# Kernel tuning notes

Measured on AMD Instinct MI355X. Metric: run time of the kernel, lower is better.

Reference implementation:

```python
import jax, jax.numpy as jnp
import numpy as np

N, K, IN, FEAT, H, OUT, E = 30000, 25, 64, 32, 128, 64, 480000


def setup_inputs() -> dict:
    key = jax.random.key(0)
    ks = jax.random.split(key, 24)
    w = lambda k, shp: (jax.random.normal(k, shp, dtype=jnp.float32) * 0.05)
    z = lambda n: jnp.zeros((n,), jnp.float32)
    return {
        "x": jax.random.normal(ks[0], (N, IN), jnp.float32),
        "dists_max": jax.random.uniform(ks[1], (N, K), jnp.float32),
        "dists_argmax": jax.random.randint(ks[2], (N, K), 0, N, jnp.int32),
        "edge_index": jax.random.randint(ks[3], (2, E), 0, N, jnp.int32),
        "train_mask": jnp.ones((E,), jnp.int32),
        # PGNN.linear_pre: in -> 32
        "w_pre": w(ks[4], (IN, FEAT)), "b_pre": z(FEAT),
        # conv_first (PGNN_layer(32, 128))
        "l1_dc_w1": w(ks[5], (1, H)), "l1_dc_b1": z(H),
        "l1_dc_w2": w(ks[6], (H, 1)), "l1_dc_b2": z(1),
        "l1_wh": w(ks[7], (2 * FEAT, H)), "l1_bh": z(H),
        "l1_wp": w(ks[8], (H, 1)), "l1_bp": z(1),
        # conv_out (PGNN_layer(128, 128))
        "l2_dc_w1": w(ks[9], (1, H)), "l2_dc_b1": z(H),
        "l2_dc_w2": w(ks[10], (H, 1)), "l2_dc_b2": z(1),
        "l2_wh": w(ks[11], (2 * H, H)), "l2_bh": z(H),
        "l2_wp": w(ks[12], (H, 1)), "l2_bp": z(1),
        # GNNModel.layers[1]: Linear(len_distmax=25 -> hidden=128)
        "w_lin": w(ks[13], (K, H)), "b_lin": z(H),
        # FeedForwardNetwork(2H -> 2H -> OUT)
        "ff_w1": w(ks[14], (2 * H, 2 * H)), "ff_b1": z(2 * H),
        "ff_w2": w(ks[15], (2 * H, OUT)), "ff_b2": z(OUT),
    }


def _nonlinear(d, w1, b1, w2, b2):
    # Nonlinear(1, H, 1) applied to dists: [N, K] -> [N, K]
    h = jax.nn.relu(d[..., None] @ w1 + b1)  # [N, K, H]
    return (h @ w2 + b2)[..., 0]


def _pgnn_layer(feat, dmax, argmax, dc_w1, dc_b1, dc_w2, dc_b2, wh, bh, wp, bp):
    d = _nonlinear(dmax, dc_w1, dc_b1, dc_w2, dc_b2)          # [N, K]
    sub = feat[argmax]                                         # gather: [N, K, F]
    self_feat = jnp.broadcast_to(feat[:, None, :], sub.shape)  # [N, K, F]
    msgs = jnp.concatenate([sub * d[..., None], self_feat], axis=-1)  # [N, K, 2F]
    msgs = jax.nn.relu(msgs @ wh + bh)                         # [N, K, H]
    out_position = (msgs @ wp + bp)[..., 0]                    # [N, K]
    out_structure = msgs.mean(axis=1)                          # [N, H]
    return out_position, out_structure


def reference(x, dists_max, dists_argmax, edge_index, train_mask,
              w_pre, b_pre,
              l1_dc_w1, l1_dc_b1, l1_dc_w2, l1_dc_b2, l1_wh, l1_bh, l1_wp, l1_bp,
              l2_dc_w1, l2_dc_b1, l2_dc_w2, l2_dc_b2, l2_wh, l2_bh, l2_wp, l2_bp,
              w_lin, b_lin, ff_w1, ff_b1, ff_w2, ff_b2):
    # PGNN (layer_num=2, feature_pre=True)
    h = x @ w_pre + b_pre                                      # [N, 32]
    _, h = _pgnn_layer(h, dists_max, dists_argmax,
                       l1_dc_w1, l1_dc_b1, l1_dc_w2, l1_dc_b2,
                       l1_wh, l1_bh, l1_wp, l1_bp)             # [N, H]
    x_pos, _ = _pgnn_layer(h, dists_max, dists_argmax,
                           l2_dc_w1, l2_dc_b1, l2_dc_w2, l2_dc_b2,
                           l2_wh, l2_bh, l2_wp, l2_bp)         # [N, K]
    # F.normalize(p=2, dim=-1) with eps=1e-12
    norm = jnp.maximum(jnp.linalg.norm(x_pos, axis=-1, keepdims=True), 1e-12)
    h = jax.nn.relu(x_pos / norm)                              # act after layer 0
    h = jax.nn.relu(h @ w_lin + b_lin)                         # layers[1] + act, [N, H]
    # get_minibatch_embeddings: select train edges, gather endpoint embeddings
    idx = np.where(np.asarray(train_mask) == 1)[0]
    ei = edge_index[:, idx]
    e = jnp.concatenate([h[ei[0]], h[ei[1]]], axis=1)          # [E_train, 2H]
    # FeedForwardNetwork
    e = jax.nn.relu(e @ ff_w1 + ff_b1)
    return e @ ff_w2 + ff_b2                                   # [E_train, OUT]
```

## Files before the change

### kernel.cpp

```cpp
#include <hip/hip_runtime.h>
#include <hip/hip_bf16.h>
#include <cmath>

#define NN 30000
#define KK 25
#define IN_F 64
#define FEAT 32
#define HH 128
#define OUTF 64
#define EE 480000
#define NPAGE 469
#define NB (8 * NPAGE)
#define LUTN 4096

typedef __attribute__((ext_vector_type(8))) _Float16 fp16x8;
typedef __attribute__((ext_vector_type(2))) _Float16 h2v;
typedef __attribute__((ext_vector_type(16))) float f32x16;

__device__ inline float u2f(unsigned u) { return __builtin_bit_cast(float, u); }
__device__ inline unsigned short f2b(float f) {
    __bf16 h = (__bf16)f;
    return __builtin_bit_cast(unsigned short, h);
}
__device__ inline unsigned short f2h(float f) {
    _Float16 h = (_Float16)f;
    return __builtin_bit_cast(unsigned short, h);
}
__device__ inline float blo(unsigned u) { return u2f(u << 16); }
__device__ inline float bhi(unsigned u) { return u2f(u & 0xffff0000u); }

__device__ inline unsigned hrelu2(unsigned a, unsigned b) {
    h2v x = __builtin_bit_cast(h2v, a);
    h2v y = __builtin_bit_cast(h2v, b);
    h2v s = x + y;
    h2v z = {(_Float16)0.f, (_Float16)0.f};
    h2v r = __builtin_elementwise_max(s, z);
    return __builtin_bit_cast(unsigned, r);
}

__device__ inline float lut_eval(const float* __restrict__ lut, float dm) {
    float tt = dm * (float)LUTN;
    int i0 = (int)tt;
    i0 = i0 < 0 ? 0 : (i0 > LUTN - 1 ? LUTN - 1 : i0);
    float f = tt - (float)i0;
    float l0 = lut[i0];
    return fmaf(lut[i0 + 1] - l0, f, l0);
}

__global__ void k_prep(const float* __restrict__ x,
                       const float* __restrict__ w_pre, const float* __restrict__ b_pre,
                       const float* __restrict__ l1wh, const float* __restrict__ l1bh,
                       const float* __restrict__ ffw2, const float* __restrict__ ffw1,
                       const float* __restrict__ l2wh,
                       const float* __restrict__ l1w1, const float* __restrict__ l1b1,
                       const float* __restrict__ l1w2, const float* __restrict__ l1b2,
                       const float* __restrict__ l2w1, const float* __restrict__ l2b1,
                       const float* __restrict__ l2w2, const float* __restrict__ l2b2,
                       unsigned* __restrict__ hist,
                       float* __restrict__ lut1, float* __restrict__ lut2,
                       unsigned short* __restrict__ xh, unsigned short* __restrict__ xl,
                       float* __restrict__ bfuse, unsigned short* __restrict__ wt,
                       unsigned short* __restrict__ wt1,
                       unsigned short* __restrict__ wt2h, unsigned short* __restrict__ wt2l,
                       unsigned short* __restrict__ wfh, unsigned short* __restrict__ wfl) {
    int gid = blockIdx.x * 256 + threadIdx.x;
    if (gid < NB) { hist[gid] = 0u; return; }
    gid -= NB;
    if (gid < 2 * (LUTN + 1)) {
        int which = gid / (LUTN + 1);
        int i = gid % (LUTN + 1);
        float dm = (float)i * (1.0f / (float)LUTN);
        const float* w1 = which ? l2w1 : l1w1;
        const float* b1 = which ? l2b1 : l1b1;
        const float* w2 = which ? l2w2 : l1w2;
        const float* b2 = which ? l2b2 : l1b2;
        float a = 0.f;
        for (int h = 0; h < HH; ++h)
            a = fmaf(fmaxf(fmaf(dm, w1[h], b1[h]), 0.f), w2[h], a);
        (which ? lut2 : lut1)[i] = a + b2[0];
        return;
    }
    gid -= 2 * (LUTN + 1);
    if (gid < NN * IN_F / 8) {
        int i = gid * 8;
        unsigned short vh[8], vl[8];
#pragma unroll
        for (int j = 0; j < 8; ++j) {
            float v = x[i + j];
            _Float16 hi = (_Float16)v;
            vh[j] = __builtin_bit_cast(unsigned short, hi);
            vl[j] = f2h((v - (float)hi) * 1024.f);
        }
        *(uint4*)(xh + i) = *(uint4*)vh;
        *(uint4*)(xl + i) = *(uint4*)vl;
        return;
    }
    gid -= NN * IN_F / 8;
    if (gid < 256) {
        int half = gid >> 7, h = gid & 127;
        const float* wh = l1wh + half * FEAT * HH + h;
        float acc = (half == 1) ? l1bh[h] : 0.f;
#pragma unroll
        for (int c = 0; c < FEAT; ++c) acc = fmaf(b_pre[c], wh[c * HH], acc);
        bfuse[gid] = acc;
    } else if (gid < 16640) {
        int i = gid - 256;
        int k = i >> 6, c = i & 63;
        wt[c * 256 + k] = f2h(ffw2[i]);
    } else if (gid < 82176) {
        int i = gid - 16640;
        int c = i >> 7, j = i & 127;
        float v = (c < 256) ? ffw1[j * 256 + c] : ffw1[(128 + j) * 256 + (c - 256)];
        wt1[c * 128 + j] = f2h(v);
    } else if (gid < 114944) {
        int i = gid - 82176;
        int c = i >> 7, j = i & 127;
        float v = (c < 128) ? l2wh[j * 128 + c] : l2wh[(128 + j) * 128 + (c - 128)];
        _Float16 hi = (_Float16)v;
        wt2h[c * 128 + j] = __builtin_bit_cast(unsigned short, hi);
        wt2l[c * 128 + j] = f2h((v - (float)hi) * 1024.f);
    } else if (gid < 131328) {
        int i = gid - 114944;
        int cc = i >> 6, j = i & 63;
        const float* wrow = w_pre + j * FEAT;
        float acc = 0.f;
#pragma unroll
        for (int c = 0; c < FEAT; ++c) {
            float wh = (cc < 128) ? l1wh[c * HH + cc] : l1wh[(FEAT + c) * HH + (cc - 128)];
            acc = fmaf(wrow[c], wh, acc);
        }
        _Float16 hi = (_Float16)acc;
        wfh[cc * 64 + j] = __builtin_bit_cast(unsigned short, hi);
        wfl[cc * 64 + j] = f2h((acc - (float)hi) * 1024.f);
    }
}

__global__ void k_dlut(const float* __restrict__ dmax, const float* __restrict__ lut1,
                       const float* __restrict__ lut2,
                       float* __restrict__ d1, float* __restrict__ d2) {
    int i = (blockIdx.x * 256 + threadIdx.x) * 4;
    if (i >= NN * KK) return;
    float4 dm = *(const float4*)(dmax + i);
    float4 o1, o2;
    o1.x = lut_eval(lut1, dm.x); o1.y = lut_eval(lut1, dm.y);
    o1.z = lut_eval(lut1, dm.z); o1.w = lut_eval(lut1, dm.w);
    o2.x = lut_eval(lut2, dm.x); o2.y = lut_eval(lut2, dm.y);
    o2.z = lut_eval(lut2, dm.z); o2.w = lut_eval(lut2, dm.w);
    *(float4*)(d1 + i) = o1;
    *(float4*)(d2 + i) = o2;
}

__global__ void k_hist(const int* __restrict__ ei, unsigned* __restrict__ hist) {
    int base = (blockIdx.x * 256 + threadIdx.x) * 8;
    if (base >= EE) return;
    int4 s0 = *(const int4*)(ei + base);
    int4 s1 = *(const int4*)(ei + base + 4);
    int4 d0 = *(const int4*)(ei + EE + base);
    int4 d1 = *(const int4*)(ei + EE + base + 4);
    int ss[8] = {s0.x, s0.y, s0.z, s0.w, s1.x, s1.y, s1.z, s1.w};
    int dd[8] = {d0.x, d0.y, d0.z, d0.w, d1.x, d1.y, d1.z, d1.w};
#pragma unroll
    for (int j = 0; j < 8; ++j) {
        int key = (ss[j] * 8 / NN) * NPAGE + (dd[j] >> 6);
        atomicAdd(&hist[key], 1u);
    }
}

__global__ __launch_bounds__(64) void k_scan(const unsigned* __restrict__ hist,
                                             unsigned* __restrict__ cursor) {
    int l = threadIdx.x;
    const int PER = 59;
    unsigned tot = 0;
    for (int j = 0; j < PER; ++j) {
        int i = l * PER + j;
        if (i < NB) tot += hist[i];
    }
    unsigned run = tot;
#pragma unroll
    for (int off = 1; off < 64; off <<= 1) {
        unsigned u = __shfl_up(run, off, 64);
        if (l >= off) run += u;
    }
    unsigned base = run - tot;
    for (int j = 0; j < PER; ++j) {
        int i = l * PER + j;
        if (i < NB) {
            cursor[i] = base;
            base += hist[i];
        }
    }
}

__global__ void k_scatter(const int* __restrict__ ei, unsigned* __restrict__ cursor,
                          uint4* __restrict__ sedge) {
    int base = (blockIdx.x * 256 + threadIdx.x) * 8;
    if (base >= EE) return;
    int4 s0 = *(const int4*)(ei + base);
    int4 s1 = *(const int4*)(ei + base + 4);
    int4 d0 = *(const int4*)(ei + EE + base);
    int4 d1 = *(const int4*)(ei + EE + base + 4);
    int ss[8] = {s0.x, s0.y, s0.z, s0.w, s1.x, s1.y, s1.z, s1.w};
    int dd[8] = {d0.x, d0.y, d0.z, d0.w, d1.x, d1.y, d1.z, d1.w};
    unsigned pp[8];
#pragma unroll
    for (int j = 0; j < 8; ++j) {
        int key = (ss[j] * 8 / NN) * NPAGE + (dd[j] >> 6);
        pp[j] = atomicAdd(&cursor[key], 1u);
    }
#pragma unroll
    for (int j = 0; j < 8; ++j)
        sedge[pp[j]] = make_uint4((unsigned)ss[j], (unsigned)dd[j], (unsigned)(base + j), 0u);
}

template <int KD>
__global__ __launch_bounds__(256) void k_nodegemm(
    const unsigned short* __restrict__ Ah, const unsigned short* __restrict__ Al,
    const unsigned short* __restrict__ Wh, const unsigned short* __restrict__ Wl,
    const float* __restrict__ gbias, const float* __restrict__ sbias,
    unsigned short* __restrict__ Gb, float* __restrict__ S) {
    int t = threadIdx.x;
    int l = t & 63, w = t >> 6;
    int c = l & 31, kh = l >> 5;
    int nb = blockIdx.x * 32;
    int na = nb + c;
    if (na >= NN) na = NN - 1;
    fp16x8 afh[KD / 16], afl[KD / 16];
#pragma unroll
    for (int kt = 0; kt < KD / 16; ++kt) {
        afh[kt] = *(const fp16x8*)(Ah + na * KD + kt * 16 + kh * 8);
        afl[kt] = *(const fp16x8*)(Al + na * KD + kt * 16 + kh * 8);
    }
    f32x16 acch0, acch1, accl0, accl1;
#pragma unroll
    for (int i = 0; i < 16; ++i) { acch0[i] = 0.f; acch1[i] = 0.f; accl0[i] = 0.f; accl1[i] = 0.f; }
    int cb0 = w * 64, cb1 = w * 64 + 32;
#pragma unroll
    for (int kt = 0; kt < KD / 16; ++kt) {
        fp16x8 b0h = *(const fp16x8*)(Wh + (cb0 + c) * KD + kt * 16 + kh * 8);
        fp16x8 b0l = *(const fp16x8*)(Wl + (cb0 + c) * KD + kt * 16 + kh * 8);
        fp16x8 b1h = *(const fp16x8*)(Wh + (cb1 + c) * KD + kt * 16 + kh * 8);
        fp16x8 b1l = *(const fp16x8*)(Wl + (cb1 + c) * KD + kt * 16 + kh * 8);
        acch0 = __builtin_amdgcn_mfma_f32_32x32x16_f16(afh[kt], b0h, acch0, 0, 0, 0);
        accl0 = __builtin_amdgcn_mfma_f32_32x32x16_f16(afh[kt], b0l, accl0, 0, 0, 0);
        accl0 = __builtin_amdgcn_mfma_f32_32x32x16_f16(afl[kt], b0h, accl0, 0, 0, 0);
        acch1 = __builtin_amdgcn_mfma_f32_32x32x16_f16(afh[kt], b1h, acch1, 0, 0, 0);
        accl1 = __builtin_amdgcn_mfma_f32_32x32x16_f16(afh[kt], b1l, accl1, 0, 0, 0);
        accl1 = __builtin_amdgcn_mfma_f32_32x32x16_f16(afl[kt], b1h, accl1, 0, 0, 0);
    }
    const float inv1024 = 1.0f / 1024.0f;
#pragma unroll
    for (int half = 0; half < 2; ++half) {
        int col = (half ? cb1 : cb0) + c;
        bool isG = col < HH;
        float gb_ = (isG && gbias) ? gbias[col] : 0.f;
        float sb_ = (!isG) ? sbias[col - HH] : 0.f;
#pragma unroll
        for (int r = 0; r < 16; ++r) {
            int row = (r & 3) + 8 * (r >> 2) + 4 * kh;
            int n = nb + row;
            float v = half ? (acch1[r] + accl1[r] * inv1024)
                           : (acch0[r] + accl0[r] * inv1024);
            if (n < NN) {
                if (isG) Gb[n * HH + col] = f2b(v + gb_);
                else S[n * HH + (col - HH)] = v + sb_;
            }
        }
    }
}

__global__ void k_layer1(const unsigned* __restrict__ G1u, const float* __restrict__ S1,
                         const float* __restrict__ d1, const int* __restrict__ amax,
                         unsigned* __restrict__ hh, unsigned* __restrict__ hl) {
    int t = threadIdx.x;
    int n = blockIdx.x * 4 + (t >> 6);
    int l = t & 63;
    float2 sv = *(const float2*)(S1 + n * HH + 2 * l);
    const int* arow = amax + n * KK;
    const float* drow = d1 + n * KK;
    unsigned gvv[KK];
#pragma unroll
    for (int k = 0; k < KK; ++k) gvv[k] = G1u[arow[k] * 64 + l];
    float dk_[KK];
#pragma unroll
    for (int k = 0; k < KK; ++k) dk_[k] = drow[k];
    float acc0 = 0.f, acc1 = 0.f;
#pragma unroll
    for (int k = 0; k < KK; ++k) {
        acc0 += fmaxf(fmaf(dk_[k], blo(gvv[k]), sv.x), 0.f);
        acc1 += fmaxf(fmaf(dk_[k], bhi(gvv[k]), sv.y), 0.f);
    }
    float a0 = acc0 * 0.04f, a1 = acc1 * 0.04f;
    _Float16 h0 = (_Float16)a0, h1v = (_Float16)a1;
    float r0 = (a0 - (float)h0) * 1024.f, r1 = (a1 - (float)h1v) * 1024.f;
    hh[n * 64 + l] = (unsigned)__builtin_bit_cast(unsigned short, h0) |
                     ((unsigned)__builtin_bit_cast(unsigned short, h1v) << 16);
    hl[n * 64 + l] = (unsigned)f2h(r0) | ((unsigned)f2h(r1) << 16);
}

__global__ __launch_bounds__(256) void k_xpos2(
    const uint2* __restrict__ G2u2, const float* __restrict__ S2,
    const float* __restrict__ d2, const int* __restrict__ amax,
    const float* __restrict__ wp, const float* __restrict__ bp,
    const float* __restrict__ wlin, const float* __restrict__ blin,
    uint2* __restrict__ hlu2) {
    int t = threadIdx.x;
    int s = t & 31;
    int n = blockIdx.x * 8 + (t >> 5);
    float4 sv = *(const float4*)(S2 + n * HH + 4 * s);
    float4 wpv = *(const float4*)(wp + 4 * s);
    const int* arow = amax + n * KK;
    const float* drow = d2 + n * KK;
    uint2 gvv[KK];
#pragma unroll
    for (int k = 0; k < KK; ++k) gvv[k] = G2u2[(size_t)arow[k] * 32 + s];
    float dk_[KK];
#pragma unroll
    for (int k = 0; k < KK; ++k) dk_[k] = drow[k];
    float v[KK];
#pragma unroll
    for (int k = 0; k < KK; ++k) {
        float d = dk_[k];
        float t0 = fmaxf(fmaf(d, blo(gvv[k].x), sv.x), 0.f);
        float t1 = fmaxf(fmaf(d, bhi(gvv[k].x), sv.y), 0.f);
        float t2 = fmaxf(fmaf(d, blo(gvv[k].y), sv.z), 0.f);
        float t3 = fmaxf(fmaf(d, bhi(gvv[k].y), sv.w), 0.f);
        v[k] = t0 * wpv.x + t1 * wpv.y + t2 * wpv.z + t3 * wpv.w;
    }
#pragma unroll
    for (int sh = 1; sh < 32; sh <<= 1) {
#pragma unroll
        for (int k = 0; k < KK; ++k) v[k] += __shfl_xor(v[k], sh, 64);
    }
    float bpv = bp[0];
    float ss = 0.f;
#pragma unroll
    for (int k = 0; k < KK; ++k) { v[k] += bpv; ss = fmaf(v[k], v[k], ss); }
    float inv = 1.0f / fmaxf(sqrtf(ss), 1e-12f);
    float4 bl = *(const float4*)(blin + 4 * s);
    float a0 = bl.x, a1 = bl.y, a2 = bl.z, a3 = bl.w;
#pragma unroll
    for (int k = 0; k < KK; ++k) {
        float xv = fmaxf(v[k], 0.f) * inv;
        float4 wl = *(const float4*)(wlin + k * HH + 4 * s);
        a0 = fmaf(xv, wl.x, a0);
        a1 = fmaf(xv, wl.y, a1);
        a2 = fmaf(xv, wl.z, a2);
        a3 = fmaf(xv, wl.w, a3);
    }
    uint2 o;
    o.x = (unsigned)f2h(fmaxf(a0, 0.f)) | ((unsigned)f2h(fmaxf(a1, 0.f)) << 16);
    o.y = (unsigned)f2h(fmaxf(a2, 0.f)) | ((unsigned)f2h(fmaxf(a3, 0.f)) << 16);
    hlu2[(size_t)n * 32 + s] = o;
}

__global__ __launch_bounds__(256) void k_ab_mfma(
    const unsigned short* __restrict__ hl16, const unsigned short* __restrict__ wt1,
    const float* __restrict__ ffb1, unsigned short* __restrict__ ab) {
    int t = threadIdx.x;
    int l = t & 63, w = t >> 6;
    int c = l & 31, kh = l >> 5;
    int nb = blockIdx.x * 32;
    int na = nb + c;
    if (na >= NN) na = NN - 1;
    fp16x8 af[8];
#pragma unroll
    for (int kt = 0; kt < 8; ++kt)
        af[kt] = *(const fp16x8*)(hl16 + na * 128 + kt * 16 + kh * 8);
    f32x16 acc[4];
#pragma unroll
    for (int g = 0; g < 4; ++g)
#pragma unroll
        for (int i = 0; i < 16; ++i) acc[g][i] = 0.f;
#pragma unroll
    for (int kt = 0; kt < 8; ++kt) {
#pragma unroll
        for (int g = 0; g < 4; ++g) {
            fp16x8 b = *(const fp16x8*)(wt1 + (w * 128 + g * 32 + c) * 128 + kt * 16 + kh * 8);
            acc[g] = __builtin_amdgcn_mfma_f32_32x32x16_f16(af[kt], b, acc[g], 0, 0, 0);
        }
    }
#pragma unroll
    for (int g = 0; g < 4; ++g) {
        int col = w * 128 + g * 32 + c;
        float bias = (col >= 256) ? ffb1[col - 256] : 0.f;
#pragma unroll
        for (int r = 0; r < 16; ++r) {
            int row = (r & 3) + 8 * (r >> 2) + 4 * kh;
            int n = nb + row;
            if (n < NN) ab[n * 512 + col] = f2h(acc[g][r] + bias);
        }
    }
}

__global__ __launch_bounds__(256, 2) void k_edge_mfma(
    const unsigned short* __restrict__ abf, const uint4* __restrict__ sedge,
    const unsigned short* __restrict__ wt, const float* __restrict__ ffb2,
    float* __restrict__ out) {
    __shared__ uint4 P[128 * 32];
    int t = threadIdx.x;
    int l = t & 63;
    int w = t >> 6;
    int c = l & 31, kh = l >> 5;

    fp16x8 wf0[16], wf1[16];
#pragma unroll
    for (int kt = 0; kt < 16; ++kt) {
        wf0[kt] = *(const fp16x8*)(wt + c * 256 + kt * 16 + kh * 8);
        wf1[kt] = *(const fp16x8*)(wt + (c + 32) * 256 + kt * 16 + kh * 8);
    }
    float bias0 = ffb2[c], bias1 = ffb2[c + 32];

    int xcd = blockIdx.x & 7;
    int slot = blockIdx.x >> 3;
    int seg = t & 31;
    int rb = t >> 5;

    for (int tl = slot; tl < NPAGE; tl += 64) {
        int tb = (xcd * NPAGE + tl) * 128;
#pragma unroll 4
        for (int r = 0; r < 16; ++r) {
            int row = r * 8 + rb;
            int pos = tb + row;
            uint4 rec = sedge[pos < EE ? pos : EE - 1];
            uint4 a = *(const uint4*)(abf + (size_t)rec.x * 512 + seg * 8);
            uint4 b = *(const uint4*)(abf + (size_t)rec.y * 512 + 256 + seg * 8);
            uint4 p;
            p.x = hrelu2(a.x, b.x);
            p.y = hrelu2(a.y, b.y);
            p.z = hrelu2(a.z, b.z);
            p.w = hrelu2(a.w, b.w);
            int col = (seg * 16) ^ ((row & 15) << 4);
            P[row * 32 + (col >> 4)] = p;
        }
        __syncthreads();
        f32x16 acc0, acc1;
#pragma unroll
        for (int i = 0; i < 16; ++i) { acc0[i] = 0.f; acc1[i] = 0.f; }
        int wrow = w * 32 + c;
        int sw = (wrow & 15) << 4;
#pragma unroll
        for (int kt = 0; kt < 16; ++kt) {
            int col = (kt * 32 + kh * 16) ^ sw;
            fp16x8 af = __builtin_bit_cast(fp16x8, P[wrow * 32 + (col >> 4)]);
            acc0 = __builtin_amdgcn_mfma_f32_32x32x16_f16(af, wf0[kt], acc0, 0, 0, 0);
            acc1 = __builtin_amdgcn_mfma_f32_32x32x16_f16(af, wf1[kt], acc1, 0, 0, 0);
        }
        int spos = tb + wrow;
        int eid = (int)sedge[spos < EE ? spos : EE - 1].z;
        int rbase = 4 * kh;
#pragma unroll
        for (int r = 0; r < 16; ++r) {
            int row = (r & 3) + 8 * (r >> 2) + rbase;
            int eidr = __shfl(eid, row, 64);
            if (tb + w * 32 + row < EE) {
                size_t o = (size_t)eidr * 64;
                out[o + c] = acc0[r] + bias0;
                out[o + 32 + c] = acc1[r] + bias1;
            }
        }
        __syncthreads();
    }
}

extern "C" void kernel_launch(void* const* d_in, const int* in_sizes, int n_in,
                              void* d_out, int out_size, void* d_ws, size_t ws_size,
                              hipStream_t stream) {
    const float* x     = (const float*)d_in[0];
    const float* dmax  = (const float*)d_in[1];
    const int*   amax  = (const int*)d_in[2];
    const int*   ei    = (const int*)d_in[3];
    const float* w_pre = (const float*)d_in[5];
    const float* b_pre = (const float*)d_in[6];
    const float* l1w1  = (const float*)d_in[7];
    const float* l1b1  = (const float*)d_in[8];
    const float* l1w2  = (const float*)d_in[9];
    const float* l1b2  = (const float*)d_in[10];
    const float* l1wh  = (const float*)d_in[11];
    const float* l1bh  = (const float*)d_in[12];
    const float* l2w1  = (const float*)d_in[15];
    const float* l2b1  = (const float*)d_in[16];
    const float* l2w2  = (const float*)d_in[17];
    const float* l2b2  = (const float*)d_in[18];
    const float* l2wh  = (const float*)d_in[19];
    const float* l2bh  = (const float*)d_in[20];
    const float* l2wp  = (const float*)d_in[21];
    const float* l2bp  = (const float*)d_in[22];
    const float* wlin  = (const float*)d_in[23];
    const float* blin  = (const float*)d_in[24];
    const float* ffw1  = (const float*)d_in[25];
    const float* ffb1  = (const float*)d_in[26];
    const float* ffw2  = (const float*)d_in[27];
    const float* ffb2  = (const float*)d_in[28];

    float* ws = (float*)d_ws;
    unsigned short* Gb = (unsigned short*)(ws + 1500000);
    float* S  = ws + 3500000;
    unsigned short* xh = (unsigned short*)(ws + 7500000);
    unsigned short* xl = (unsigned short*)(ws + 8500000);
    unsigned* hhp = (unsigned*)(ws + 9500000);
    unsigned* hlp = (unsigned*)(ws + 11500000);
    unsigned short* hl16 = (unsigned short*)(ws + 13500000);
    uint4* sedge = (uint4*)(ws + 15500000);
    unsigned short* wfh = (unsigned short*)(ws + 17500000);
    unsigned short* wfl = (unsigned short*)(ws + 17510000);
    float* bfuse = ws + 17520000;
    unsigned short* wt = (unsigned short*)(ws + 17530000);
    unsigned short* wt1 = (unsigned short*)(ws + 17540000);
    unsigned short* wt2h = (unsigned short*)(ws + 17580000);
    unsigned short* wt2l = (unsigned short*)(ws + 17600000);
    unsigned* hist = (unsigned*)(ws + 17620000);
    unsigned* cursor = (unsigned*)(ws + 17630000);
    float* lut1 = ws + 17640000;
    float* lut2 = ws + 17645000;
    float* d1 = ws + 18000000;
    float* d2 = ws + 18750000;
    unsigned short* ab = (unsigned short*)ws;
    float* out = (float*)d_out;

    k_prep<<<1498, 256, 0, stream>>>(x, w_pre, b_pre, l1wh, l1bh, ffw2, ffw1, l2wh,
                                     l1w1, l1b1, l1w2, l1b2, l2w1, l2b1, l2w2, l2b2,
                                     hist, lut1, lut2, xh, xl,
                                     bfuse, wt, wt1, wt2h, wt2l, wfh, wfl);
    k_dlut<<<(NN * KK / 4 + 255) / 256, 256, 0, stream>>>(dmax, lut1, lut2, d1, d2);

    k_hist<<<(EE / 8 + 255) / 256, 256, 0, stream>>>(ei, hist);
    k_scan<<<1, 64, 0, stream>>>(hist, cursor);
    k_scatter<<<(EE / 8 + 255) / 256, 256, 0, stream>>>(ei, cursor, sedge);

    k_nodegemm<IN_F><<<938, 256, 0, stream>>>(xh, xl, wfh, wfl, bfuse, bfuse + 128, Gb, S);
    k_layer1<<<NN / 4, 256, 0, stream>>>((const unsigned*)Gb, S, d1, amax, hhp, hlp);
    k_nodegemm<HH><<<938, 256, 0, stream>>>((const unsigned short*)hhp,
                                            (const unsigned short*)hlp, wt2h, wt2l,
                                            nullptr, l2bh, Gb, S);
    k_xpos2<<<NN / 8, 256, 0, stream>>>((const uint2*)Gb, S, d2, amax,
                                        l2wp, l2bp, wlin, blin, (uint2*)hl16);
    k_ab_mfma<<<938, 256, 0, stream>>>(hl16, wt1, ffb1, ab);

    k_edge_mfma<<<512, 256, 0, stream>>>(ab, sedge, wt, ffb2, out);
}
```

Before: 316.4 us.

## Fuse dlut and hist launches, widen layer1 gathers, halve edge tile size

The distance-LUT evaluation and the edge histogram now run in one kernel launch, which removes one launch and its gap. k_layer1 now gives each thread four channels through uint2 gathers with 8 nodes per block, instead of two channels and 4 nodes, so fewer but wider memory transactions are issued. k_edge_mfma now processes 64-edge tiles with 128-thread blocks, twice as many blocks and half the shared memory. This aims for better occupancy and load balance, at the cost of less reuse of the per-block weight fragments loaded into registers.

```diff
diff --git a/kernel.cpp b/kernel.cpp
--- a/kernel.cpp
+++ b/kernel.cpp
@@ -12,6 +12,7 @@
 #define NPAGE 469
 #define NB (8 * NPAGE)
 #define LUTN 4096
+#define NT64 938
 
 typedef __attribute__((ext_vector_type(8))) _Float16 fp16x8;
 typedef __attribute__((ext_vector_type(2))) _Float16 h2v;
@@ -135,30 +136,32 @@
     }
 }
 
-__global__ void k_dlut(const float* __restrict__ dmax, const float* __restrict__ lut1,
-                       const float* __restrict__ lut2,
-                       float* __restrict__ d1, float* __restrict__ d2) {
-    int i = (blockIdx.x * 256 + threadIdx.x) * 4;
-    if (i >= NN * KK) return;
-    float4 dm = *(const float4*)(dmax + i);
-    float4 o1, o2;
-    o1.x = lut_eval(lut1, dm.x); o1.y = lut_eval(lut1, dm.y);
-    o1.z = lut_eval(lut1, dm.z); o1.w = lut_eval(lut1, dm.w);
-    o2.x = lut_eval(lut2, dm.x); o2.y = lut_eval(lut2, dm.y);
-    o2.z = lut_eval(lut2, dm.z); o2.w = lut_eval(lut2, dm.w);
-    *(float4*)(d1 + i) = o1;
-    *(float4*)(d2 + i) = o2;
-}
-
-__global__ void k_hist(const int* __restrict__ ei, unsigned* __restrict__ hist) {
-    int base = (blockIdx.x * 256 + threadIdx.x) * 8;
+#define DL_N (NN * KK / 4)
+__global__ void k_dlut_hist(const float* __restrict__ dmax, const float* __restrict__ lut1,
+                            const float* __restrict__ lut2,
+                            float* __restrict__ d1, float* __restrict__ d2,
+                            const int* __restrict__ ei, unsigned* __restrict__ hist) {
+    int gid = blockIdx.x * 256 + threadIdx.x;
+    if (gid < DL_N) {
+        int i = gid * 4;
+        float4 dm = *(const float4*)(dmax + i);
+        float4 o1, o2;
+        o1.x = lut_eval(lut1, dm.x); o1.y = lut_eval(lut1, dm.y);
+        o1.z = lut_eval(lut1, dm.z); o1.w = lut_eval(lut1, dm.w);
+        o2.x = lut_eval(lut2, dm.x); o2.y = lut_eval(lut2, dm.y);
+        o2.z = lut_eval(lut2, dm.z); o2.w = lut_eval(lut2, dm.w);
+        *(float4*)(d1 + i) = o1;
+        *(float4*)(d2 + i) = o2;
+        return;
+    }
+    int base = (gid - DL_N) * 8;
     if (base >= EE) return;
     int4 s0 = *(const int4*)(ei + base);
     int4 s1 = *(const int4*)(ei + base + 4);
-    int4 d0 = *(const int4*)(ei + EE + base);
-    int4 d1 = *(const int4*)(ei + EE + base + 4);
+    int4 dd0 = *(const int4*)(ei + EE + base);
+    int4 dd1 = *(const int4*)(ei + EE + base + 4);
     int ss[8] = {s0.x, s0.y, s0.z, s0.w, s1.x, s1.y, s1.z, s1.w};
-    int dd[8] = {d0.x, d0.y, d0.z, d0.w, d1.x, d1.y, d1.z, d1.w};
+    int dd[8] = {dd0.x, dd0.y, dd0.z, dd0.w, dd1.x, dd1.y, dd1.z, dd1.w};
 #pragma unroll
     for (int j = 0; j < 8; ++j) {
         int key = (ss[j] * 8 / NN) * NPAGE + (dd[j] >> 6);
@@ -268,33 +271,43 @@
     }
 }
 
-__global__ void k_layer1(const unsigned* __restrict__ G1u, const float* __restrict__ S1,
+__global__ void k_layer1(const uint2* __restrict__ G1u2, const float* __restrict__ S1,
                          const float* __restrict__ d1, const int* __restrict__ amax,
-                         unsigned* __restrict__ hh, unsigned* __restrict__ hl) {
+                         uint2* __restrict__ hh, uint2* __restrict__ hl) {
     int t = threadIdx.x;
-    int n = blockIdx.x * 4 + (t >> 6);
-    int l = t & 63;
-    float2 sv = *(const float2*)(S1 + n * HH + 2 * l);
+    int s = t & 31;
+    int n = blockIdx.x * 8 + (t >> 5);
+    float4 sv = *(const float4*)(S1 + n * HH + 4 * s);
     const int* arow = amax + n * KK;
     const float* drow = d1 + n * KK;
-    unsigned gvv[KK];
-#pragma unroll
-    for (int k = 0; k < KK; ++k) gvv[k] = G1u[arow[k] * 64 + l];
+    uint2 gvv[KK];
+#pragma unroll
+    for (int k = 0; k < KK; ++k) gvv[k] = G1u2[(size_t)arow[k] * 32 + s];
     float dk_[KK];
 #pragma unroll
     for (int k = 0; k < KK; ++k) dk_[k] = drow[k];
-    float acc0 = 0.f, acc1 = 0.f;
+    float a0 = 0.f, a1 = 0.f, a2 = 0.f, a3 = 0.f;
 #pragma unroll
     for (int k = 0; k < KK; ++k) {
-        acc0 += fmaxf(fmaf(dk_[k], blo(gvv[k]), sv.x), 0.f);
-        acc1 += fmaxf(fmaf(dk_[k], bhi(gvv[k]), sv.y), 0.f);
-    }
-    float a0 = acc0 * 0.04f, a1 = acc1 * 0.04f;
-    _Float16 h0 = (_Float16)a0, h1v = (_Float16)a1;
-    float r0 = (a0 - (float)h0) * 1024.f, r1 = (a1 - (float)h1v) * 1024.f;
-    hh[n * 64 + l] = (unsigned)__builtin_bit_cast(unsigned short, h0) |
-                     ((unsigned)__builtin_bit_cast(unsigned short, h1v) << 16);
-    hl[n * 64 + l] = (unsigned)f2h(r0) | ((unsigned)f2h(r1) << 16);
+        float d = dk_[k];
+        a0 += fmaxf(fmaf(d, blo(gvv[k].x), sv.x), 0.f);
+        a1 += fmaxf(fmaf(d, bhi(gvv[k].x), sv.y), 0.f);
+        a2 += fmaxf(fmaf(d, blo(gvv[k].y), sv.z), 0.f);
+        a3 += fmaxf(fmaf(d, bhi(gvv[k].y), sv.w), 0.f);
+    }
+    a0 *= 0.04f; a1 *= 0.04f; a2 *= 0.04f; a3 *= 0.04f;
+    _Float16 h0 = (_Float16)a0, h1v = (_Float16)a1, h2v_ = (_Float16)a2, h3 = (_Float16)a3;
+    uint2 oh, ol;
+    oh.x = (unsigned)__builtin_bit_cast(unsigned short, h0) |
+           ((unsigned)__builtin_bit_cast(unsigned short, h1v) << 16);
+    oh.y = (unsigned)__builtin_bit_cast(unsigned short, h2v_) |
+           ((unsigned)__builtin_bit_cast(unsigned short, h3) << 16);
+    ol.x = (unsigned)f2h((a0 - (float)h0) * 1024.f) |
+           ((unsigned)f2h((a1 - (float)h1v) * 1024.f) << 16);
+    ol.y = (unsigned)f2h((a2 - (float)h2v_) * 1024.f) |
+           ((unsigned)f2h((a3 - (float)h3) * 1024.f) << 16);
+    hh[(size_t)n * 32 + s] = oh;
+    hl[(size_t)n * 32 + s] = ol;
 }
 
 __global__ __launch_bounds__(256) void k_xpos2(
@@ -392,11 +405,11 @@
     }
 }
 
-__global__ __launch_bounds__(256, 2) void k_edge_mfma(
+__global__ __launch_bounds__(128, 2) void k_edge_mfma(
     const unsigned short* __restrict__ abf, const uint4* __restrict__ sedge,
     const unsigned short* __restrict__ wt, const float* __restrict__ ffb2,
     float* __restrict__ out) {
-    __shared__ uint4 P[128 * 32];
+    __shared__ uint4 P[64 * 32];
     int t = threadIdx.x;
     int l = t & 63;
     int w = t >> 6;
@@ -415,11 +428,11 @@
     int seg = t & 31;
     int rb = t >> 5;
 
-    for (int tl = slot; tl < NPAGE; tl += 64) {
-        int tb = (xcd * NPAGE + tl) * 128;
+    for (int tl = slot; tl < NT64; tl += 128) {
+        int tb = (xcd * NT64 + tl) * 64;
 #pragma unroll 4
-        for (int r = 0; r < 16; ++r) {
-            int row = r * 8 + rb;
+        for (int it = 0; it < 16; ++it) {
+            int row = it * 4 + rb;
             int pos = tb + row;
             uint4 rec = sedge[pos < EE ? pos : EE - 1];
             uint4 a = *(const uint4*)(abf + (size_t)rec.x * 512 + seg * 8);
@@ -521,14 +534,14 @@
                                      l1w1, l1b1, l1w2, l1b2, l2w1, l2b1, l2w2, l2b2,
                                      hist, lut1, lut2, xh, xl,
                                      bfuse, wt, wt1, wt2h, wt2l, wfh, wfl);
-    k_dlut<<<(NN * KK / 4 + 255) / 256, 256, 0, stream>>>(dmax, lut1, lut2, d1, d2);
-
-    k_hist<<<(EE / 8 + 255) / 256, 256, 0, stream>>>(ei, hist);
+    k_dlut_hist<<<(DL_N + EE / 8 + 255) / 256, 256, 0, stream>>>(
+        dmax, lut1, lut2, d1, d2, ei, hist);
     k_scan<<<1, 64, 0, stream>>>(hist, cursor);
     k_scatter<<<(EE / 8 + 255) / 256, 256, 0, stream>>>(ei, cursor, sedge);
 
     k_nodegemm<IN_F><<<938, 256, 0, stream>>>(xh, xl, wfh, wfl, bfuse, bfuse + 128, Gb, S);
-    k_layer1<<<NN / 4, 256, 0, stream>>>((const unsigned*)Gb, S, d1, amax, hhp, hlp);
+    k_layer1<<<NN / 8, 256, 0, stream>>>((const uint2*)Gb, S, d1, amax,
+                                         (uint2*)hhp, (uint2*)hlp);
     k_nodegemm<HH><<<938, 256, 0, stream>>>((const unsigned short*)hhp,
                                             (const unsigned short*)hlp, wt2h, wt2l,
                                             nullptr, l2bh, Gb, S);
@@ -536,5 +549,5 @@
                                         l2wp, l2bp, wlin, blin, (uint2*)hl16);
     k_ab_mfma<<<938, 256, 0, stream>>>(hl16, wt1, ffb1, ab);
 
-    k_edge_mfma<<<512, 256, 0, stream>>>(ab, sedge, wt, ffb2, out);
-}
+    k_edge_mfma<<<1024, 128, 0, stream>>>(ab, sedge, wt, ffb2, out);
+}
```

Measured after the change: 316.7 us. No clear change (+0.1%).
